# Performance work log

Hardware: AMD Instinct MI355X
Metric: run time of the kernel (lower is better)

## Reference

```python
import jax, jax.numpy as jnp
import numpy as np

N_EMBD = 1024
N_EXPERTS = 8
TOP_K = 2
CAPACITY_FACTOR = 1.25


def setup_inputs() -> dict:
    key = jax.random.key(0)
    ks = jax.random.split(key, 8)
    B, T, C, E, H = 8, 2048, N_EMBD, N_EXPERTS, 4 * N_EMBD
    w = lambda k, shape: jax.random.normal(k, shape, jnp.float32) * 0.02
    return {
        "x": jax.random.normal(ks[0], (B, T, C), jnp.float32),
        # router MLP: C -> 4C -> 4C -> E
        "rW1": w(ks[1], (C, H)), "rb1": jnp.zeros((H,), jnp.float32),
        "rW2": w(ks[2], (H, H)), "rb2": jnp.zeros((H,), jnp.float32),
        "rW3": w(ks[3], (H, E)), "rb3": jnp.zeros((E,), jnp.float32),
        # per-expert FFN: C -> 4C -> C (one expert per rank in the original)
        "eW1": w(ks[4], (E, C, H)), "eb1": jnp.zeros((E, H), jnp.float32),
        "eW2": w(ks[5], (E, H, C)), "eb2": jnp.zeros((E, C), jnp.float32),
    }


def reference(x, rW1, rb1, rW2, rb2, rW3, rb3, eW1, eb1, eW2, eb2):
    B, T, C = x.shape
    E = rb3.shape[0]
    k = TOP_K
    capacity = int(T / E * CAPACITY_FACTOR)  # per (row, expert) capacity

    # --- router (dropout = identity in eval) ---
    h = jax.nn.relu(x @ rW1 + rb1)
    h = jax.nn.relu(h @ rW2 + rb2)
    scales = jax.nn.softmax(h @ rW3 + rb3, axis=-1)            # [B,T,E]
    topk_scales, topk_experts = jax.lax.top_k(scales, k)       # [B,T,k]

    # --- dispatch: position of each assignment within its (row, expert) group,
    # in (t, slot) order, matching the source's nonzero() ordering ---
    e_flat = topk_experts.reshape(B, T * k)                    # [B,T*k]
    onehot = jax.nn.one_hot(e_flat, E, dtype=jnp.int32)        # [B,T*k,E]
    pos_excl = jnp.cumsum(onehot, axis=1) - onehot             # exclusive prefix count
    pos = jnp.take_along_axis(pos_excl, e_flat[..., None], axis=-1)[..., 0]
    keep = pos < capacity                                      # over-capacity tokens dropped (-> padding_val=0)
    pos_c = jnp.where(keep, pos, capacity)                     # OOB slot -> dropped by scatter

    b_idx = jnp.broadcast_to(jnp.arange(B)[:, None], (B, T * k))
    x_rep = jnp.repeat(x, k, axis=1)                           # [B,T*k,C], token copied per top-k slot

    dispatched = jnp.zeros((E, B, capacity, C), x.dtype)
    dispatched = dispatched.at[e_flat, b_idx, pos_c].set(
        jnp.where(keep[..., None], x_rep, 0.0), mode="drop")

    # --- per-expert FFN on capacity-padded batches ---
    hh = jax.nn.relu(jnp.einsum("ebnc,ech->ebnh", dispatched, eW1) + eb1[:, None, None, :])
    eout = jnp.einsum("ebnh,ehc->ebnc", hh, eW2) + eb2[:, None, None, :]

    # --- combine: gather back, zero dropped slots, weight by router gates ---
    gathered = eout[e_flat, b_idx, pos_c]                      # clamped gather; masked next
    gathered = jnp.where(keep[..., None], gathered, 0.0).reshape(B, T, k, C)
    out = jnp.sum(topk_scales[..., None] * gathered, axis=2)   # [B,T,C]
    return out
```

## Files before the change

### kernel.cpp

```cpp
#include <hip/hip_runtime.h>
#include <hip/hip_bf16.h>

#define BDIM 8
#define TDIM 2048
#define CDIM 1024
#define HDIM 4096
#define EDIM 8
#define CAPACITY 320
#define MTOK (BDIM*TDIM)
#define MCHUNK 2048
#define NCHUNKS (MTOK/MCHUNK)
#define EROWS (BDIM*CAPACITY)
#define NROWS (EDIM*EROWS)

typedef __attribute__((ext_vector_type(8))) short bf16x8;
typedef __attribute__((ext_vector_type(8))) _Float16 f16x8;
typedef __attribute__((ext_vector_type(4))) float f32x4;

__device__ __forceinline__ unsigned short f2bf(float f){
    __hip_bfloat16 h = __float2bfloat16(f);
    return *reinterpret_cast<unsigned short*>(&h);
}

__device__ __forceinline__ void f32_split(float v, unsigned short& h, unsigned short& l){
    _Float16 hh = (_Float16)v;
    float r = v - (float)hh;
    _Float16 ll = (_Float16)r;
    h = __builtin_bit_cast(unsigned short, hh);
    l = __builtin_bit_cast(unsigned short, ll);
}

__device__ __forceinline__ void glds16(const unsigned short* g, unsigned short* l){
    __builtin_amdgcn_global_load_lds(
        (const __attribute__((address_space(1))) void*)g,
        (__attribute__((address_space(3))) void*)l,
        16, 0, 0);
}

__device__ __forceinline__ void xcd_tile(int& bx, int& by){
    int nbx = gridDim.x, nby = gridDim.y;
    int nwg = nbx * nby;
    int orig = blockIdx.y * nbx + blockIdx.x;
    int wg = orig;
    if ((nwg & 7) == 0){
        int cpx = nwg >> 3;
        wg = (orig & 7) * cpx + (orig >> 3);
    }
    bx = wg % nbx;
    by = wg / nbx;
}

__global__ __launch_bounds__(256) void transpose_convert(
    const float* __restrict__ in, unsigned short* __restrict__ out, int R, int Ccol)
{
    int z = blockIdx.z;
    in  += (size_t)z * R * Ccol;
    out += (size_t)z * R * Ccol;
    __shared__ float tile[32][33];
    int r0 = blockIdx.y * 32, c0 = blockIdx.x * 32;
    int tid = threadIdx.x;
    int lr = tid >> 5, lc = tid & 31;
    #pragma unroll
    for (int it = 0; it < 4; it++)
        tile[it*8 + lr][lc] = in[(size_t)(r0 + it*8 + lr) * Ccol + c0 + lc];
    __syncthreads();
    #pragma unroll
    for (int it = 0; it < 4; it++){
        float v = tile[lc][it*8 + lr];
        out[(size_t)(c0 + it*8 + lr) * R + r0 + lc] = f2bf(v);
    }
}

__global__ __launch_bounds__(256) void transpose_split(
    const float* __restrict__ in, unsigned short* __restrict__ hi,
    unsigned short* __restrict__ lo, int R, int Ccol)
{
    __shared__ float tile[32][33];
    int r0 = blockIdx.y * 32, c0 = blockIdx.x * 32;
    int tid = threadIdx.x;
    int lr = tid >> 5, lc = tid & 31;
    #pragma unroll
    for (int it = 0; it < 4; it++)
        tile[it*8 + lr][lc] = in[(size_t)(r0 + it*8 + lr) * Ccol + c0 + lc];
    __syncthreads();
    #pragma unroll
    for (int it = 0; it < 4; it++){
        float v = tile[lc][it*8 + lr];
        unsigned short h, l;
        f32_split(v, h, l);
        size_t o = (size_t)(c0 + it*8 + lr) * R + r0 + lc;
        hi[o] = h; lo[o] = l;
    }
}

__global__ __launch_bounds__(256) void split_f16(
    const float* __restrict__ in, unsigned short* __restrict__ hi,
    unsigned short* __restrict__ lo, size_t n4)
{
    size_t i = (size_t)blockIdx.x * 256 + threadIdx.x;
    if (i >= n4) return;
    float4 v = ((const float4*)in)[i];
    ushort4 h, l;
    f32_split(v.x, h.x, l.x);
    f32_split(v.y, h.y, l.y);
    f32_split(v.z, h.z, l.z);
    f32_split(v.w, h.w, l.w);
    ((ushort4*)hi)[i] = h;
    ((ushort4*)lo)[i] = l;
}

__global__ __launch_bounds__(256) void gemm_f16x3_128(
    const unsigned short* __restrict__ Ahi, const unsigned short* __restrict__ Alo,
    const unsigned short* __restrict__ Bthi, const unsigned short* __restrict__ Btlo,
    const float* __restrict__ bias, void* __restrict__ outA, void* __restrict__ outB,
    int M, int N, int K, int mode)
{
    __shared__ unsigned short AsH[2][128*32];
    __shared__ unsigned short AsL[2][128*32];
    __shared__ unsigned short BsH[2][128*32];
    __shared__ unsigned short BsL[2][128*32];
    int tid = threadIdx.x;
    int bx, by; xcd_tile(bx, by);
    int m0 = bx * 128, n0 = by * 128;
    int lane = tid & 63, w = tid >> 6;
    int wm = w & 1, wn = w >> 1;
    int l15 = lane & 15, quad = lane >> 4;

    f32x4 acc[4][4];
    #pragma unroll
    for (int i = 0; i < 4; i++)
        #pragma unroll
        for (int j = 0; j < 4; j++){ acc[i][j].x=0.f; acc[i][j].y=0.f; acc[i][j].z=0.f; acc[i][j].w=0.f; }

    const unsigned short *pAh[2], *pAl[2], *pBh[2], *pBl[2];
    int wo[2];
    #pragma unroll
    for (int i = 0; i < 2; i++){
        int r0  = w*32 + i*16;
        int row = r0 + (lane >> 2);
        int ks  = ((lane & 3) * 8) ^ ((row & 6) << 2);
        pAh[i] = Ahi  + (size_t)(m0 + row) * K + ks;
        pAl[i] = Alo  + (size_t)(m0 + row) * K + ks;
        pBh[i] = Bthi + (size_t)(n0 + row) * K + ks;
        pBl[i] = Btlo + (size_t)(n0 + row) * K + ks;
        wo[i]  = r0 * 32;
    }

    int roA[4], roB[4];
    #pragma unroll
    for (int t = 0; t < 4; t++){
        int ra = wm*64 + t*16 + l15;
        roA[t] = (ra*64 + quad*16) ^ ((ra & 6) << 3);
        int rb = wn*64 + t*16 + l15;
        roB[t] = (rb*64 + quad*16) ^ ((rb & 6) << 3);
    }

    #pragma unroll
    for (int i = 0; i < 2; i++){
        glds16(pAh[i], &AsH[0][wo[i]]);
        glds16(pAl[i], &AsL[0][wo[i]]);
        glds16(pBh[i], &BsH[0][wo[i]]);
        glds16(pBl[i], &BsL[0][wo[i]]);
    }
    __syncthreads();

    int nt = K >> 5;
    int cur = 0;
    for (int t = 0; t < nt; t++){
        if (t + 1 < nt){
            int ko = (t + 1) * 32;
            #pragma unroll
            for (int i = 0; i < 2; i++){
                glds16(pAh[i] + ko, &AsH[cur^1][wo[i]]);
                glds16(pAl[i] + ko, &AsL[cur^1][wo[i]]);
                glds16(pBh[i] + ko, &BsH[cur^1][wo[i]]);
                glds16(pBl[i] + ko, &BsL[cur^1][wo[i]]);
            }
        }
        f16x8 ah[4], al[4], bh[4], bl[4];
        #pragma unroll
        for (int t4 = 0; t4 < 4; t4++){
            ah[t4] = *(const f16x8*)((const char*)AsH[cur] + roA[t4]);
            al[t4] = *(const f16x8*)((const char*)AsL[cur] + roA[t4]);
            bh[t4] = *(const f16x8*)((const char*)BsH[cur] + roB[t4]);
            bl[t4] = *(const f16x8*)((const char*)BsL[cur] + roB[t4]);
        }
        __builtin_amdgcn_s_setprio(1);
        #pragma unroll
        for (int mt = 0; mt < 4; mt++)
            #pragma unroll
            for (int nt2 = 0; nt2 < 4; nt2++){
                acc[mt][nt2] = __builtin_amdgcn_mfma_f32_16x16x32_f16(ah[mt], bh[nt2], acc[mt][nt2], 0, 0, 0);
                acc[mt][nt2] = __builtin_amdgcn_mfma_f32_16x16x32_f16(ah[mt], bl[nt2], acc[mt][nt2], 0, 0, 0);
                acc[mt][nt2] = __builtin_amdgcn_mfma_f32_16x16x32_f16(al[mt], bh[nt2], acc[mt][nt2], 0, 0, 0);
            }
        __builtin_amdgcn_s_setprio(0);
        __syncthreads();
        cur ^= 1;
    }

    #pragma unroll
    for (int mt = 0; mt < 4; mt++)
        #pragma unroll
        for (int nt2 = 0; nt2 < 4; nt2++){
            int mb = m0 + wm*64 + mt*16 + quad*4;
            int n  = n0 + wn*64 + nt2*16 + l15;
            float bz = bias[n];
            #pragma unroll
            for (int r = 0; r < 4; r++){
                float v = fmaxf(acc[mt][nt2][r] + bz, 0.f);
                int m = mb + r;
                if (mode == 0){
                    unsigned short h, l;
                    f32_split(v, h, l);
                    ((unsigned short*)outA)[(size_t)m * N + n] = h;
                    ((unsigned short*)outB)[(size_t)m * N + n] = l;
                } else {
                    ((float*)outA)[(size_t)m * N + n] = v;
                }
            }
        }
}

__global__ __launch_bounds__(256) void gemm_bf16_128(
    const unsigned short* __restrict__ A, const unsigned short* __restrict__ Bt,
    const float* __restrict__ bias, void* __restrict__ outv,
    int M, int N, int K, int mode)
{
    __shared__ unsigned short As[2][128*32];
    __shared__ unsigned short Bs[2][128*32];
    int tid = threadIdx.x;
    int bx, by; xcd_tile(bx, by);
    int m0 = bx * 128, n0 = by * 128;
    int lane = tid & 63, w = tid >> 6;
    int wm = w & 1, wn = w >> 1;
    int l15 = lane & 15, quad = lane >> 4;

    f32x4 acc[4][4];
    #pragma unroll
    for (int i = 0; i < 4; i++)
        #pragma unroll
        for (int j = 0; j < 4; j++){ acc[i][j].x=0.f; acc[i][j].y=0.f; acc[i][j].z=0.f; acc[i][j].w=0.f; }

    const unsigned short *pA[2], *pB[2];
    int wo[2];
    #pragma unroll
    for (int i = 0; i < 2; i++){
        int r0  = w*32 + i*16;
        int row = r0 + (lane >> 2);
        int ks  = ((lane & 3) * 8) ^ ((row & 6) << 2);
        pA[i] = A  + (size_t)(m0 + row) * K + ks;
        pB[i] = Bt + (size_t)(n0 + row) * K + ks;
        wo[i] = r0 * 32;
    }

    int roA[4], roB[4];
    #pragma unroll
    for (int t = 0; t < 4; t++){
        int ra = wm*64 + t*16 + l15;
        roA[t] = (ra*64 + quad*16) ^ ((ra & 6) << 3);
        int rb = wn*64 + t*16 + l15;
        roB[t] = (rb*64 + quad*16) ^ ((rb & 6) << 3);
    }

    #pragma unroll
    for (int i = 0; i < 2; i++){
        glds16(pA[i], &As[0][wo[i]]);
        glds16(pB[i], &Bs[0][wo[i]]);
    }
    __syncthreads();

    int nt = K >> 5;
    int cur = 0;
    for (int t = 0; t < nt; t++){
        if (t + 1 < nt){
            int ko = (t + 1) * 32;
            #pragma unroll
            for (int i = 0; i < 2; i++){
                glds16(pA[i] + ko, &As[cur^1][wo[i]]);
                glds16(pB[i] + ko, &Bs[cur^1][wo[i]]);
            }
        }
        bf16x8 af[4], bf[4];
        #pragma unroll
        for (int t4 = 0; t4 < 4; t4++){
            af[t4] = *(const bf16x8*)((const char*)As[cur] + roA[t4]);
            bf[t4] = *(const bf16x8*)((const char*)Bs[cur] + roB[t4]);
        }
        __builtin_amdgcn_s_setprio(1);
        #pragma unroll
        for (int mt = 0; mt < 4; mt++)
            #pragma unroll
            for (int nt2 = 0; nt2 < 4; nt2++)
                acc[mt][nt2] = __builtin_amdgcn_mfma_f32_16x16x32_bf16(af[mt], bf[nt2], acc[mt][nt2], 0, 0, 0);
        __builtin_amdgcn_s_setprio(0);
        __syncthreads();
        cur ^= 1;
    }

    #pragma unroll
    for (int mt = 0; mt < 4; mt++)
        #pragma unroll
        for (int nt2 = 0; nt2 < 4; nt2++){
            int mb = m0 + wm*64 + mt*16 + quad*4;
            int n  = n0 + wn*64 + nt2*16 + l15;
            float bz = bias[n];
            #pragma unroll
            for (int r = 0; r < 4; r++){
                float v = acc[mt][nt2][r] + bz;
                int m = mb + r;
                if (mode == 0){
                    v = fmaxf(v, 0.f);
                    ((unsigned short*)outv)[(size_t)m * N + n] = f2bf(v);
                } else {
                    ((float*)outv)[(size_t)m * N + n] = v;
                }
            }
        }
}

__global__ __launch_bounds__(256) void router_head(
    const float* __restrict__ h2, const float* __restrict__ W3,
    const float* __restrict__ b3, int tokBase,
    int* __restrict__ top2e, float* __restrict__ top2s)
{
    int tid = threadIdx.x;
    int tloc = blockIdx.x * 32 + (tid >> 3);
    int e = tid & 7;
    const float* hrow = h2 + (size_t)tloc * HDIM;
    float acc = 0.f;
    for (int k = 0; k < HDIM; k += 4){
        float4 h = *(const float4*)(hrow + k);
        acc = fmaf(h.x, W3[(k+0)*8 + e], acc);
        acc = fmaf(h.y, W3[(k+1)*8 + e], acc);
        acc = fmaf(h.z, W3[(k+2)*8 + e], acc);
        acc = fmaf(h.w, W3[(k+3)*8 + e], acc);
    }
    float logit = acc + b3[e];
    __shared__ float lg[32][8];
    lg[tid >> 3][e] = logit;
    __syncthreads();
    if (tid < 32){
        double l[8];
        double mx = -1e300;
        for (int i = 0; i < 8; i++){ l[i] = (double)lg[tid][i]; if (l[i] > mx) mx = l[i]; }
        double ex[8]; double s = 0.0;
        for (int i = 0; i < 8; i++){ ex[i] = exp(l[i] - mx); s += ex[i]; }
        double b1v = -1.0, b2v = -1.0; int e1 = 0, e2 = 0;
        for (int i = 0; i < 8; i++){
            double v = ex[i];
            if (v > b1v){ b2v = b1v; e2 = e1; b1v = v; e1 = i; }
            else if (v > b2v){ b2v = v; e2 = i; }
        }
        int gt = tokBase + blockIdx.x * 32 + tid;
        top2e[gt*2 + 0] = e1;
        top2e[gt*2 + 1] = e2;
        top2s[gt*2 + 0] = (float)(b1v / s);
        top2s[gt*2 + 1] = (float)(b2v / s);
    }
}

__global__ __launch_bounds__(256) void scan_dispatch(
    const int* __restrict__ top2e, int* __restrict__ slot_row, int* __restrict__ row2tok)
{
    int b = blockIdx.x;
    int tid = threadIdx.x;
    __shared__ int cnt[256][8];
    int base = b * (TDIM * 2);
    int i0 = tid * 16;
    int c[8];
    #pragma unroll
    for (int e = 0; e < 8; e++) c[e] = 0;
    for (int j = 0; j < 16; j++){
        int e = top2e[base + i0 + j];
        c[e]++;
    }
    #pragma unroll
    for (int e = 0; e < 8; e++) cnt[tid][e] = c[e];
    __syncthreads();
    if (tid < 8){
        int run = 0;
        for (int t = 0; t < 256; t++){ int v = cnt[t][tid]; cnt[t][tid] = run; run += v; }
    }
    __syncthreads();
    int offs[8];
    #pragma unroll
    for (int e = 0; e < 8; e++) offs[e] = cnt[tid][e];
    for (int j = 0; j < 16; j++){
        int i = i0 + j;
        int e = top2e[base + i];
        int pos = offs[e]++;
        int r = (pos < CAPACITY) ? ((e * BDIM + b) * CAPACITY + pos) : -1;
        slot_row[base + i] = r;
        if (r >= 0) row2tok[r] = b * TDIM + (i >> 1);
    }
}

__global__ __launch_bounds__(256) void gather_rows(
    const float* __restrict__ x, const int* __restrict__ row2tok,
    unsigned short* __restrict__ Xe)
{
    int r = blockIdx.x;
    int tid = threadIdx.x;
    int tok = row2tok[r];
    unsigned short* dst = Xe + (size_t)r * CDIM + tid * 4;
    if (tok >= 0){
        float4 v = *(const float4*)(x + (size_t)tok * CDIM + tid * 4);
        ushort4 o;
        o.x = f2bf(v.x); o.y = f2bf(v.y); o.z = f2bf(v.z); o.w = f2bf(v.w);
        *(ushort4*)dst = o;
    } else {
        ushort4 o; o.x = o.y = o.z = o.w = 0;
        *(ushort4*)dst = o;
    }
}

__global__ __launch_bounds__(256) void combine(
    const float* __restrict__ eout, const int* __restrict__ slot_row,
    const float* __restrict__ top2s, float* __restrict__ out)
{
    int gt = blockIdx.x;
    int b = gt >> 11, t = gt & (TDIM - 1);
    int i = b * (TDIM * 2) + t * 2;
    int r1 = slot_row[i], r2 = slot_row[i + 1];
    float s1 = top2s[gt*2 + 0], s2 = top2s[gt*2 + 1];
    int c = threadIdx.x * 4;
    float4 acc; acc.x = acc.y = acc.z = acc.w = 0.f;
    if (r1 >= 0){
        float4 v = *(const float4*)(eout + (size_t)r1 * CDIM + c);
        acc.x = fmaf(s1, v.x, acc.x); acc.y = fmaf(s1, v.y, acc.y);
        acc.z = fmaf(s1, v.z, acc.z); acc.w = fmaf(s1, v.w, acc.w);
    }
    if (r2 >= 0){
        float4 v = *(const float4*)(eout + (size_t)r2 * CDIM + c);
        acc.x = fmaf(s2, v.x, acc.x); acc.y = fmaf(s2, v.y, acc.y);
        acc.z = fmaf(s2, v.z, acc.z); acc.w = fmaf(s2, v.w, acc.w);
    }
    *(float4*)(out + (size_t)gt * CDIM + c) = acc;
}

extern "C" void kernel_launch(void* const* d_in, const int* in_sizes, int n_in,
                              void* d_out, int out_size, void* d_ws, size_t ws_size,
                              hipStream_t stream)
{
    const float* x   = (const float*)d_in[0];
    const float* rW1 = (const float*)d_in[1];
    const float* rb1 = (const float*)d_in[2];
    const float* rW2 = (const float*)d_in[3];
    const float* rb2 = (const float*)d_in[4];
    const float* rW3 = (const float*)d_in[5];
    const float* rb3 = (const float*)d_in[6];
    const float* eW1 = (const float*)d_in[7];
    const float* eb1 = (const float*)d_in[8];
    const float* eW2 = (const float*)d_in[9];
    const float* eb2 = (const float*)d_in[10];
    float* out = (float*)d_out;

    char* p = (char*)d_ws;
    auto alloc = [&](size_t bytes) -> void* {
        void* q = (void*)p;
        p += (bytes + 255) & ~(size_t)255;
        return q;
    };
    int*            top2e = (int*)alloc((size_t)MTOK * 2 * 4);
    float*          top2s = (float*)alloc((size_t)MTOK * 2 * 4);
    int*            slotr = (int*)alloc((size_t)BDIM * TDIM * 2 * 4);
    int*            r2tok = (int*)alloc((size_t)NROWS * 4);
    float*          eout  = (float*)alloc((size_t)NROWS * CDIM * 4);
    char* ubase = p;

    unsigned short* Xhi   = (unsigned short*)alloc((size_t)MTOK * CDIM * 2);
    unsigned short* Xlo   = (unsigned short*)alloc((size_t)MTOK * CDIM * 2);
    unsigned short* W1thi = (unsigned short*)alloc((size_t)HDIM * CDIM * 2);
    unsigned short* W1tlo = (unsigned short*)alloc((size_t)HDIM * CDIM * 2);
    unsigned short* W2thi = (unsigned short*)alloc((size_t)HDIM * HDIM * 2);
    unsigned short* W2tlo = (unsigned short*)alloc((size_t)HDIM * HDIM * 2);
    unsigned short* H1hi  = (unsigned short*)alloc((size_t)MCHUNK * HDIM * 2);
    unsigned short* H1lo  = (unsigned short*)alloc((size_t)MCHUNK * HDIM * 2);
    float*          h2c   = (float*)alloc((size_t)MCHUNK * HDIM * 4);

    p = ubase;
    unsigned short* Xe    = (unsigned short*)alloc((size_t)NROWS * CDIM * 2);
    unsigned short* He    = (unsigned short*)alloc((size_t)EROWS * HDIM * 2);
    unsigned short* eW1t  = (unsigned short*)alloc((size_t)EDIM * HDIM * CDIM * 2);
    unsigned short* eW2t  = (unsigned short*)alloc((size_t)EDIM * CDIM * HDIM * 2);

    split_f16<<<(MTOK * CDIM / 4 + 255) / 256, 256, 0, stream>>>(x, Xhi, Xlo, (size_t)MTOK * CDIM / 4);
    transpose_split<<<dim3(HDIM/32, CDIM/32), 256, 0, stream>>>(rW1, W1thi, W1tlo, CDIM, HDIM);
    transpose_split<<<dim3(HDIM/32, HDIM/32), 256, 0, stream>>>(rW2, W2thi, W2tlo, HDIM, HDIM);

    for (int mc = 0; mc < NCHUNKS; mc++){
        const unsigned short* xh = Xhi + (size_t)mc * MCHUNK * CDIM;
        const unsigned short* xl = Xlo + (size_t)mc * MCHUNK * CDIM;
        gemm_f16x3_128<<<dim3(MCHUNK/128, HDIM/128), 256, 0, stream>>>(
            xh, xl, W1thi, W1tlo, rb1, (void*)H1hi, (void*)H1lo, MCHUNK, HDIM, CDIM, 0);
        gemm_f16x3_128<<<dim3(MCHUNK/128, HDIM/128), 256, 0, stream>>>(
            H1hi, H1lo, W2thi, W2tlo, rb2, (void*)h2c, nullptr, MCHUNK, HDIM, HDIM, 1);
        router_head<<<MCHUNK/32, 256, 0, stream>>>(h2c, rW3, rb3, mc * MCHUNK, top2e, top2s);
    }

    hipMemsetAsync(r2tok, 0xFF, (size_t)NROWS * 4, stream);
    scan_dispatch<<<BDIM, 256, 0, stream>>>(top2e, slotr, r2tok);
    gather_rows<<<NROWS, 256, 0, stream>>>(x, r2tok, Xe);

    transpose_convert<<<dim3(HDIM/32, CDIM/32, EDIM), 256, 0, stream>>>(eW1, eW1t, CDIM, HDIM);
    transpose_convert<<<dim3(CDIM/32, HDIM/32, EDIM), 256, 0, stream>>>(eW2, eW2t, HDIM, CDIM);

    for (int e = 0; e < EDIM; e++){
        const unsigned short* Ae  = Xe   + (size_t)e * EROWS * CDIM;
        const unsigned short* B1  = eW1t + (size_t)e * HDIM * CDIM;
        const unsigned short* B2  = eW2t + (size_t)e * CDIM * HDIM;
        const float*          bz1 = eb1  + (size_t)e * HDIM;
        const float*          bz2 = eb2  + (size_t)e * CDIM;
        float*                Oe  = eout + (size_t)e * EROWS * CDIM;
        gemm_bf16_128<<<dim3(EROWS/128, HDIM/128), 256, 0, stream>>>(Ae, B1, bz1, (void*)He, EROWS, HDIM, CDIM, 0);
        gemm_bf16_128<<<dim3(EROWS/128, CDIM/128), 256, 0, stream>>>(He, B2, bz2, (void*)Oe, EROWS, CDIM, HDIM, 1);
    }

    combine<<<MTOK, 256, 0, stream>>>(eout, slotr, top2s, out);
}
```

Baseline: 4.051 ms.

## Enlarge router GEMM tiles to 256x256, chunk x splitting, batch expert pairs

The router's split-fp16 GEMM moves from 128x128 tiles with 256 threads to 256x256 tiles with 512 threads and 128KB of dynamic LDS. This raises arithmetic intensity and cuts global traffic per FLOP. The router chunk size doubles, and the x hi/lo split now runs per chunk into a smaller buffer instead of over the whole input. Expert FFN GEMMs now launch two experts per grid through a z dimension, which halves launch count and fills more CUs, at the cost of a doubled hidden buffer. The larger tile raises register pressure (acc[8][4]) and occupancy may drop.

```diff
diff --git a/kernel.cpp b/kernel.cpp
--- a/kernel.cpp
+++ b/kernel.cpp
@@ -8,7 +8,7 @@
 #define EDIM 8
 #define CAPACITY 320
 #define MTOK (BDIM*TDIM)
-#define MCHUNK 2048
+#define MCHUNK 4096
 #define NCHUNKS (MTOK/MCHUNK)
 #define EROWS (BDIM*CAPACITY)
 #define NROWS (EDIM*EROWS)
@@ -109,26 +109,23 @@
     ((ushort4*)lo)[i] = l;
 }
 
-__global__ __launch_bounds__(256) void gemm_f16x3_128(
+__global__ __launch_bounds__(512, 2) void gemm_f16x3_256(
     const unsigned short* __restrict__ Ahi, const unsigned short* __restrict__ Alo,
     const unsigned short* __restrict__ Bthi, const unsigned short* __restrict__ Btlo,
     const float* __restrict__ bias, void* __restrict__ outA, void* __restrict__ outB,
     int M, int N, int K, int mode)
 {
-    __shared__ unsigned short AsH[2][128*32];
-    __shared__ unsigned short AsL[2][128*32];
-    __shared__ unsigned short BsH[2][128*32];
-    __shared__ unsigned short BsL[2][128*32];
+    extern __shared__ unsigned short lds[];
     int tid = threadIdx.x;
     int bx, by; xcd_tile(bx, by);
-    int m0 = bx * 128, n0 = by * 128;
+    int m0 = bx * 256, n0 = by * 256;
     int lane = tid & 63, w = tid >> 6;
-    int wm = w & 1, wn = w >> 1;
+    int wm = w >> 2, wn = w & 3;
     int l15 = lane & 15, quad = lane >> 4;
 
-    f32x4 acc[4][4];
-    #pragma unroll
-    for (int i = 0; i < 4; i++)
+    f32x4 acc[8][4];
+    #pragma unroll
+    for (int i = 0; i < 8; i++)
         #pragma unroll
         for (int j = 0; j < 4; j++){ acc[i][j].x=0.f; acc[i][j].y=0.f; acc[i][j].z=0.f; acc[i][j].w=0.f; }
 
@@ -136,7 +133,7 @@
     int wo[2];
     #pragma unroll
     for (int i = 0; i < 2; i++){
-        int r0  = w*32 + i*16;
+        int r0  = i*128 + w*16;
         int row = r0 + (lane >> 2);
         int ks  = ((lane & 3) * 8) ^ ((row & 6) << 2);
         pAh[i] = Ahi  + (size_t)(m0 + row) * K + ks;
@@ -146,69 +143,77 @@
         wo[i]  = r0 * 32;
     }
 
-    int roA[4], roB[4];
+    int roA[8], roB[4];
+    #pragma unroll
+    for (int t = 0; t < 8; t++){
+        int ra = wm*128 + t*16 + l15;
+        roA[t] = (ra*64 + quad*16) ^ ((ra & 6) << 3);
+    }
     #pragma unroll
     for (int t = 0; t < 4; t++){
-        int ra = wm*64 + t*16 + l15;
-        roA[t] = (ra*64 + quad*16) ^ ((ra & 6) << 3);
         int rb = wn*64 + t*16 + l15;
         roB[t] = (rb*64 + quad*16) ^ ((rb & 6) << 3);
     }
 
+    unsigned short* seg[8];
+    #pragma unroll
+    for (int s = 0; s < 8; s++) seg[s] = lds + s * 8192;
+
     #pragma unroll
     for (int i = 0; i < 2; i++){
-        glds16(pAh[i], &AsH[0][wo[i]]);
-        glds16(pAl[i], &AsL[0][wo[i]]);
-        glds16(pBh[i], &BsH[0][wo[i]]);
-        glds16(pBl[i], &BsL[0][wo[i]]);
-    }
-    __syncthreads();
-
-    int nt = K >> 5;
+        glds16(pAh[i], seg[0] + wo[i]);
+        glds16(pAl[i], seg[2] + wo[i]);
+        glds16(pBh[i], seg[4] + wo[i]);
+        glds16(pBl[i], seg[6] + wo[i]);
+    }
+    __syncthreads();
+
+    int ntk = K >> 5;
     int cur = 0;
-    for (int t = 0; t < nt; t++){
-        if (t + 1 < nt){
+    for (int t = 0; t < ntk; t++){
+        if (t + 1 < ntk){
             int ko = (t + 1) * 32;
             #pragma unroll
             for (int i = 0; i < 2; i++){
-                glds16(pAh[i] + ko, &AsH[cur^1][wo[i]]);
-                glds16(pAl[i] + ko, &AsL[cur^1][wo[i]]);
-                glds16(pBh[i] + ko, &BsH[cur^1][wo[i]]);
-                glds16(pBl[i] + ko, &BsL[cur^1][wo[i]]);
+                glds16(pAh[i] + ko, seg[0 + (cur^1)] + wo[i]);
+                glds16(pAl[i] + ko, seg[2 + (cur^1)] + wo[i]);
+                glds16(pBh[i] + ko, seg[4 + (cur^1)] + wo[i]);
+                glds16(pBl[i] + ko, seg[6 + (cur^1)] + wo[i]);
             }
         }
-        f16x8 ah[4], al[4], bh[4], bl[4];
-        #pragma unroll
-        for (int t4 = 0; t4 < 4; t4++){
-            ah[t4] = *(const f16x8*)((const char*)AsH[cur] + roA[t4]);
-            al[t4] = *(const f16x8*)((const char*)AsL[cur] + roA[t4]);
-            bh[t4] = *(const f16x8*)((const char*)BsH[cur] + roB[t4]);
-            bl[t4] = *(const f16x8*)((const char*)BsL[cur] + roB[t4]);
+        f16x8 bh[4], bl[4];
+        #pragma unroll
+        for (int nt = 0; nt < 4; nt++){
+            bh[nt] = *(const f16x8*)((const char*)seg[4 + cur] + roB[nt]);
+            bl[nt] = *(const f16x8*)((const char*)seg[6 + cur] + roB[nt]);
         }
         __builtin_amdgcn_s_setprio(1);
         #pragma unroll
-        for (int mt = 0; mt < 4; mt++)
+        for (int mt = 0; mt < 8; mt++){
+            f16x8 amh = *(const f16x8*)((const char*)seg[0 + cur] + roA[mt]);
+            f16x8 aml = *(const f16x8*)((const char*)seg[2 + cur] + roA[mt]);
             #pragma unroll
-            for (int nt2 = 0; nt2 < 4; nt2++){
-                acc[mt][nt2] = __builtin_amdgcn_mfma_f32_16x16x32_f16(ah[mt], bh[nt2], acc[mt][nt2], 0, 0, 0);
-                acc[mt][nt2] = __builtin_amdgcn_mfma_f32_16x16x32_f16(ah[mt], bl[nt2], acc[mt][nt2], 0, 0, 0);
-                acc[mt][nt2] = __builtin_amdgcn_mfma_f32_16x16x32_f16(al[mt], bh[nt2], acc[mt][nt2], 0, 0, 0);
+            for (int nt = 0; nt < 4; nt++){
+                acc[mt][nt] = __builtin_amdgcn_mfma_f32_16x16x32_f16(amh, bh[nt], acc[mt][nt], 0, 0, 0);
+                acc[mt][nt] = __builtin_amdgcn_mfma_f32_16x16x32_f16(amh, bl[nt], acc[mt][nt], 0, 0, 0);
+                acc[mt][nt] = __builtin_amdgcn_mfma_f32_16x16x32_f16(aml, bh[nt], acc[mt][nt], 0, 0, 0);
             }
+        }
         __builtin_amdgcn_s_setprio(0);
         __syncthreads();
         cur ^= 1;
     }
 
     #pragma unroll
-    for (int mt = 0; mt < 4; mt++)
-        #pragma unroll
-        for (int nt2 = 0; nt2 < 4; nt2++){
-            int mb = m0 + wm*64 + mt*16 + quad*4;
-            int n  = n0 + wn*64 + nt2*16 + l15;
+    for (int mt = 0; mt < 8; mt++)
+        #pragma unroll
+        for (int nt = 0; nt < 4; nt++){
+            int mb = m0 + wm*128 + mt*16 + quad*4;
+            int n  = n0 + wn*64 + nt*16 + l15;
             float bz = bias[n];
             #pragma unroll
             for (int r = 0; r < 4; r++){
-                float v = fmaxf(acc[mt][nt2][r] + bz, 0.f);
+                float v = fmaxf(acc[mt][nt][r] + bz, 0.f);
                 int m = mb + r;
                 if (mode == 0){
                     unsigned short h, l;
@@ -225,10 +230,15 @@
 __global__ __launch_bounds__(256) void gemm_bf16_128(
     const unsigned short* __restrict__ A, const unsigned short* __restrict__ Bt,
     const float* __restrict__ bias, void* __restrict__ outv,
-    int M, int N, int K, int mode)
+    int M, int N, int K, int mode,
+    size_t zsA, size_t zsB, size_t zsb, size_t zsO)
 {
     __shared__ unsigned short As[2][128*32];
     __shared__ unsigned short Bs[2][128*32];
+    int z = blockIdx.z;
+    A    += (size_t)z * zsA;
+    Bt   += (size_t)z * zsB;
+    bias += (size_t)z * zsb;
     int tid = threadIdx.x;
     int bx, by; xcd_tile(bx, by);
     int m0 = bx * 128, n0 = by * 128;
@@ -270,10 +280,10 @@
     }
     __syncthreads();
 
-    int nt = K >> 5;
+    int ntk = K >> 5;
     int cur = 0;
-    for (int t = 0; t < nt; t++){
-        if (t + 1 < nt){
+    for (int t = 0; t < ntk; t++){
+        if (t + 1 < ntk){
             int ko = (t + 1) * 32;
             #pragma unroll
             for (int i = 0; i < 2; i++){
@@ -311,9 +321,9 @@
                 int m = mb + r;
                 if (mode == 0){
                     v = fmaxf(v, 0.f);
-                    ((unsigned short*)outv)[(size_t)m * N + n] = f2bf(v);
+                    ((unsigned short*)outv)[(size_t)z * zsO + (size_t)m * N + n] = f2bf(v);
                 } else {
-                    ((float*)outv)[(size_t)m * N + n] = v;
+                    ((float*)outv)[(size_t)z * zsO + (size_t)m * N + n] = v;
                 }
             }
         }
@@ -456,6 +466,13 @@
     const float* eb2 = (const float*)d_in[10];
     float* out = (float*)d_out;
 
+    static bool attr_done = false;
+    if (!attr_done){
+        hipFuncSetAttribute((const void*)gemm_f16x3_256,
+                            hipFuncAttributeMaxDynamicSharedMemorySize, 131072);
+        attr_done = true;
+    }
+
     char* p = (char*)d_ws;
     auto alloc = [&](size_t bytes) -> void* {
         void* q = (void*)p;
@@ -469,8 +486,8 @@
     float*          eout  = (float*)alloc((size_t)NROWS * CDIM * 4);
     char* ubase = p;
 
-    unsigned short* Xhi   = (unsigned short*)alloc((size_t)MTOK * CDIM * 2);
-    unsigned short* Xlo   = (unsigned short*)alloc((size_t)MTOK * CDIM * 2);
+    unsigned short* Xchi  = (unsigned short*)alloc((size_t)MCHUNK * CDIM * 2);
+    unsigned short* Xclo  = (unsigned short*)alloc((size_t)MCHUNK * CDIM * 2);
     unsigned short* W1thi = (unsigned short*)alloc((size_t)HDIM * CDIM * 2);
     unsigned short* W1tlo = (unsigned short*)alloc((size_t)HDIM * CDIM * 2);
     unsigned short* W2thi = (unsigned short*)alloc((size_t)HDIM * HDIM * 2);
@@ -481,20 +498,19 @@
 
     p = ubase;
     unsigned short* Xe    = (unsigned short*)alloc((size_t)NROWS * CDIM * 2);
-    unsigned short* He    = (unsigned short*)alloc((size_t)EROWS * HDIM * 2);
+    unsigned short* He    = (unsigned short*)alloc((size_t)2 * EROWS * HDIM * 2);
     unsigned short* eW1t  = (unsigned short*)alloc((size_t)EDIM * HDIM * CDIM * 2);
     unsigned short* eW2t  = (unsigned short*)alloc((size_t)EDIM * CDIM * HDIM * 2);
 
-    split_f16<<<(MTOK * CDIM / 4 + 255) / 256, 256, 0, stream>>>(x, Xhi, Xlo, (size_t)MTOK * CDIM / 4);
     transpose_split<<<dim3(HDIM/32, CDIM/32), 256, 0, stream>>>(rW1, W1thi, W1tlo, CDIM, HDIM);
     transpose_split<<<dim3(HDIM/32, HDIM/32), 256, 0, stream>>>(rW2, W2thi, W2tlo, HDIM, HDIM);
 
     for (int mc = 0; mc < NCHUNKS; mc++){
-        const unsigned short* xh = Xhi + (size_t)mc * MCHUNK * CDIM;
-        const unsigned short* xl = Xlo + (size_t)mc * MCHUNK * CDIM;
-        gemm_f16x3_128<<<dim3(MCHUNK/128, HDIM/128), 256, 0, stream>>>(
-            xh, xl, W1thi, W1tlo, rb1, (void*)H1hi, (void*)H1lo, MCHUNK, HDIM, CDIM, 0);
-        gemm_f16x3_128<<<dim3(MCHUNK/128, HDIM/128), 256, 0, stream>>>(
+        split_f16<<<(MCHUNK * CDIM / 4 + 255) / 256, 256, 0, stream>>>(
+            x + (size_t)mc * MCHUNK * CDIM, Xchi, Xclo, (size_t)MCHUNK * CDIM / 4);
+        gemm_f16x3_256<<<dim3(MCHUNK/256, HDIM/256), 512, 131072, stream>>>(
+            Xchi, Xclo, W1thi, W1tlo, rb1, (void*)H1hi, (void*)H1lo, MCHUNK, HDIM, CDIM, 0);
+        gemm_f16x3_256<<<dim3(MCHUNK/256, HDIM/256), 512, 131072, stream>>>(
             H1hi, H1lo, W2thi, W2tlo, rb2, (void*)h2c, nullptr, MCHUNK, HDIM, HDIM, 1);
         router_head<<<MCHUNK/32, 256, 0, stream>>>(h2c, rW3, rb3, mc * MCHUNK, top2e, top2s);
     }
@@ -506,15 +522,18 @@
     transpose_convert<<<dim3(HDIM/32, CDIM/32, EDIM), 256, 0, stream>>>(eW1, eW1t, CDIM, HDIM);
     transpose_convert<<<dim3(CDIM/32, HDIM/32, EDIM), 256, 0, stream>>>(eW2, eW2t, HDIM, CDIM);
 
-    for (int e = 0; e < EDIM; e++){
-        const unsigned short* Ae  = Xe   + (size_t)e * EROWS * CDIM;
-        const unsigned short* B1  = eW1t + (size_t)e * HDIM * CDIM;
-        const unsigned short* B2  = eW2t + (size_t)e * CDIM * HDIM;
-        const float*          bz1 = eb1  + (size_t)e * HDIM;
-        const float*          bz2 = eb2  + (size_t)e * CDIM;
-        float*                Oe  = eout + (size_t)e * EROWS * CDIM;
-        gemm_bf16_128<<<dim3(EROWS/128, HDIM/128), 256, 0, stream>>>(Ae, B1, bz1, (void*)He, EROWS, HDIM, CDIM, 0);
-        gemm_bf16_128<<<dim3(EROWS/128, CDIM/128), 256, 0, stream>>>(He, B2, bz2, (void*)Oe, EROWS, CDIM, HDIM, 1);
+    for (int g = 0; g < EDIM/2; g++){
+        int e0 = g * 2;
+        gemm_bf16_128<<<dim3(EROWS/128, HDIM/128, 2), 256, 0, stream>>>(
+            Xe + (size_t)e0 * EROWS * CDIM, eW1t + (size_t)e0 * HDIM * CDIM,
+            eb1 + (size_t)e0 * HDIM, (void*)He,
+            EROWS, HDIM, CDIM, 0,
+            (size_t)EROWS * CDIM, (size_t)HDIM * CDIM, (size_t)HDIM, (size_t)EROWS * HDIM);
+        gemm_bf16_128<<<dim3(EROWS/128, CDIM/128, 2), 256, 0, stream>>>(
+            He, eW2t + (size_t)e0 * CDIM * HDIM,
+            eb2 + (size_t)e0 * CDIM, (void*)(eout + (size_t)e0 * EROWS * CDIM),
+            EROWS, CDIM, HDIM, 1,
+            (size_t)EROWS * HDIM, (size_t)CDIM * HDIM, (size_t)CDIM, (size_t)EROWS * CDIM);
     }
 
     combine<<<MTOK, 256, 0, stream>>>(eout, slotr, top2s, out);
```

Result: faster. 3.552 ms (-12.3%).

## Batch two experts per GEMM launch and enlarge router chunk

Applied to the files above, without the earlier changes.

Expert FFN GEMMs now process two experts per launch via blockIdx.z strides, doubling grid size to fill more CUs. Router chunk size doubles to 4096 tokens, and the fp16 split of x is done per chunk into a smaller buffer instead of all up front. This raises GPU occupancy for small-grid GEMMs at the cost of a larger hidden buffer and intermediate workspace.

```diff
diff --git a/kernel.cpp b/kernel.cpp
--- a/kernel.cpp
+++ b/kernel.cpp
@@ -8,7 +8,7 @@
 #define EDIM 8
 #define CAPACITY 320
 #define MTOK (BDIM*TDIM)
-#define MCHUNK 2048
+#define MCHUNK 4096
 #define NCHUNKS (MTOK/MCHUNK)
 #define EROWS (BDIM*CAPACITY)
 #define NROWS (EDIM*EROWS)
@@ -164,10 +164,10 @@
     }
     __syncthreads();
 
-    int nt = K >> 5;
+    int ntk = K >> 5;
     int cur = 0;
-    for (int t = 0; t < nt; t++){
-        if (t + 1 < nt){
+    for (int t = 0; t < ntk; t++){
+        if (t + 1 < ntk){
             int ko = (t + 1) * 32;
             #pragma unroll
             for (int i = 0; i < 2; i++){
@@ -225,10 +225,15 @@
 __global__ __launch_bounds__(256) void gemm_bf16_128(
     const unsigned short* __restrict__ A, const unsigned short* __restrict__ Bt,
     const float* __restrict__ bias, void* __restrict__ outv,
-    int M, int N, int K, int mode)
+    int M, int N, int K, int mode,
+    size_t zsA, size_t zsB, size_t zsb, size_t zsO)
 {
     __shared__ unsigned short As[2][128*32];
     __shared__ unsigned short Bs[2][128*32];
+    int z = blockIdx.z;
+    A    += (size_t)z * zsA;
+    Bt   += (size_t)z * zsB;
+    bias += (size_t)z * zsb;
     int tid = threadIdx.x;
     int bx, by; xcd_tile(bx, by);
     int m0 = bx * 128, n0 = by * 128;
@@ -270,10 +275,10 @@
     }
     __syncthreads();
 
-    int nt = K >> 5;
+    int ntk = K >> 5;
     int cur = 0;
-    for (int t = 0; t < nt; t++){
-        if (t + 1 < nt){
+    for (int t = 0; t < ntk; t++){
+        if (t + 1 < ntk){
             int ko = (t + 1) * 32;
             #pragma unroll
             for (int i = 0; i < 2; i++){
@@ -311,9 +316,9 @@
                 int m = mb + r;
                 if (mode == 0){
                     v = fmaxf(v, 0.f);
-                    ((unsigned short*)outv)[(size_t)m * N + n] = f2bf(v);
+                    ((unsigned short*)outv)[(size_t)z * zsO + (size_t)m * N + n] = f2bf(v);
                 } else {
-                    ((float*)outv)[(size_t)m * N + n] = v;
+                    ((float*)outv)[(size_t)z * zsO + (size_t)m * N + n] = v;
                 }
             }
         }
@@ -469,8 +474,8 @@
     float*          eout  = (float*)alloc((size_t)NROWS * CDIM * 4);
     char* ubase = p;
 
-    unsigned short* Xhi   = (unsigned short*)alloc((size_t)MTOK * CDIM * 2);
-    unsigned short* Xlo   = (unsigned short*)alloc((size_t)MTOK * CDIM * 2);
+    unsigned short* Xchi  = (unsigned short*)alloc((size_t)MCHUNK * CDIM * 2);
+    unsigned short* Xclo  = (unsigned short*)alloc((size_t)MCHUNK * CDIM * 2);
     unsigned short* W1thi = (unsigned short*)alloc((size_t)HDIM * CDIM * 2);
     unsigned short* W1tlo = (unsigned short*)alloc((size_t)HDIM * CDIM * 2);
     unsigned short* W2thi = (unsigned short*)alloc((size_t)HDIM * HDIM * 2);
@@ -481,19 +486,18 @@
 
     p = ubase;
     unsigned short* Xe    = (unsigned short*)alloc((size_t)NROWS * CDIM * 2);
-    unsigned short* He    = (unsigned short*)alloc((size_t)EROWS * HDIM * 2);
+    unsigned short* He    = (unsigned short*)alloc((size_t)2 * EROWS * HDIM * 2);
     unsigned short* eW1t  = (unsigned short*)alloc((size_t)EDIM * HDIM * CDIM * 2);
     unsigned short* eW2t  = (unsigned short*)alloc((size_t)EDIM * CDIM * HDIM * 2);
 
-    split_f16<<<(MTOK * CDIM / 4 + 255) / 256, 256, 0, stream>>>(x, Xhi, Xlo, (size_t)MTOK * CDIM / 4);
     transpose_split<<<dim3(HDIM/32, CDIM/32), 256, 0, stream>>>(rW1, W1thi, W1tlo, CDIM, HDIM);
     transpose_split<<<dim3(HDIM/32, HDIM/32), 256, 0, stream>>>(rW2, W2thi, W2tlo, HDIM, HDIM);
 
     for (int mc = 0; mc < NCHUNKS; mc++){
-        const unsigned short* xh = Xhi + (size_t)mc * MCHUNK * CDIM;
-        const unsigned short* xl = Xlo + (size_t)mc * MCHUNK * CDIM;
+        split_f16<<<(MCHUNK * CDIM / 4 + 255) / 256, 256, 0, stream>>>(
+            x + (size_t)mc * MCHUNK * CDIM, Xchi, Xclo, (size_t)MCHUNK * CDIM / 4);
         gemm_f16x3_128<<<dim3(MCHUNK/128, HDIM/128), 256, 0, stream>>>(
-            xh, xl, W1thi, W1tlo, rb1, (void*)H1hi, (void*)H1lo, MCHUNK, HDIM, CDIM, 0);
+            Xchi, Xclo, W1thi, W1tlo, rb1, (void*)H1hi, (void*)H1lo, MCHUNK, HDIM, CDIM, 0);
         gemm_f16x3_128<<<dim3(MCHUNK/128, HDIM/128), 256, 0, stream>>>(
             H1hi, H1lo, W2thi, W2tlo, rb2, (void*)h2c, nullptr, MCHUNK, HDIM, HDIM, 1);
         router_head<<<MCHUNK/32, 256, 0, stream>>>(h2c, rW3, rb3, mc * MCHUNK, top2e, top2s);
@@ -506,15 +510,18 @@
     transpose_convert<<<dim3(HDIM/32, CDIM/32, EDIM), 256, 0, stream>>>(eW1, eW1t, CDIM, HDIM);
     transpose_convert<<<dim3(CDIM/32, HDIM/32, EDIM), 256, 0, stream>>>(eW2, eW2t, HDIM, CDIM);
 
-    for (int e = 0; e < EDIM; e++){
-        const unsigned short* Ae  = Xe   + (size_t)e * EROWS * CDIM;
-        const unsigned short* B1  = eW1t + (size_t)e * HDIM * CDIM;
-        const unsigned short* B2  = eW2t + (size_t)e * CDIM * HDIM;
-        const float*          bz1 = eb1  + (size_t)e * HDIM;
-        const float*          bz2 = eb2  + (size_t)e * CDIM;
-        float*                Oe  = eout + (size_t)e * EROWS * CDIM;
-        gemm_bf16_128<<<dim3(EROWS/128, HDIM/128), 256, 0, stream>>>(Ae, B1, bz1, (void*)He, EROWS, HDIM, CDIM, 0);
-        gemm_bf16_128<<<dim3(EROWS/128, CDIM/128), 256, 0, stream>>>(He, B2, bz2, (void*)Oe, EROWS, CDIM, HDIM, 1);
+    for (int g = 0; g < EDIM/2; g++){
+        int e0 = g * 2;
+        gemm_bf16_128<<<dim3(EROWS/128, HDIM/128, 2), 256, 0, stream>>>(
+            Xe + (size_t)e0 * EROWS * CDIM, eW1t + (size_t)e0 * HDIM * CDIM,
+            eb1 + (size_t)e0 * HDIM, (void*)He,
+            EROWS, HDIM, CDIM, 0,
+            (size_t)EROWS * CDIM, (size_t)HDIM * CDIM, (size_t)HDIM, (size_t)EROWS * HDIM);
+        gemm_bf16_128<<<dim3(EROWS/128, CDIM/128, 2), 256, 0, stream>>>(
+            He, eW2t + (size_t)e0 * CDIM * HDIM,
+            eb2 + (size_t)e0 * CDIM, (void*)(eout + (size_t)e0 * EROWS * CDIM),
+            EROWS, CDIM, HDIM, 1,
+            (size_t)EROWS * HDIM, (size_t)CDIM * HDIM, (size_t)CDIM, (size_t)EROWS * CDIM);
     }
 
     combine<<<MTOK, 256, 0, stream>>>(eout, slotr, top2s, out);
```

After: 3.531 ms. 1.15x faster.
